# Performance work log

Hardware: AMD Instinct MI355X
Metric: run time of the kernel (lower is better)

Reference implementation:

```python
import jax, jax.numpy as jnp
import numpy as np

N_LAST = 4096  # power of two; K=1 path of get_hadK


def fwht(x):
    """Fast Walsh-Hadamard transform along the last dim, normalized by 1/sqrt(n).
    Matches QuaRot matmul_hadU butterfly recursion (K=1, power-of-two n)."""
    n = x.shape[-1]
    y = x.reshape(-1, n, 1)  # (B, n, 1)
    while y.shape[1] > 1:
        y = y.reshape(y.shape[0], y.shape[1] // 2, 2, y.shape[2])
        a = y[:, :, 0, :]
        b = y[:, :, 1, :]
        # butterfly: interleave (a+b, a-b) back into the trailing dim
        y = jnp.concatenate([a + b, a - b], axis=-1)  # (B, m/2, 2k)
    return y.reshape(x.shape) * np.float32(1.0 / np.sqrt(n))


def setup_inputs() -> dict:
    key = jax.random.key(0)
    x = jax.random.normal(key, (4, 2048, N_LAST), dtype=jnp.float32)
    return {"x": x}


def reference(x) -> jnp.ndarray:
    # HadamardTransform.forward with do_rotate=True
    dtype = x.dtype
    return fwht(x).astype(dtype)
```

## Files before the change

kernel.cpp:

```cpp
#include <hip/hip_runtime.h>


constexpr int N = 4096;
constexpr int LDS_STRIDE = 17;

__device__ __forceinline__ void wht16(float v[16]) {
#pragma unroll
    for (int m = 1; m < 16; m <<= 1) {
#pragma unroll
        for (int g = 0; g < 16; g += 2 * m) {
#pragma unroll
            for (int k = 0; k < m; ++k) {
                float a = v[g + k];
                float b = v[g + k + m];
                v[g + k]     = a + b;
                v[g + k + m] = a - b;
            }
        }
    }
}

__global__ __launch_bounds__(256, 8) void fwht4096_kernel(const float* __restrict__ in,
                                                          float* __restrict__ out) {
    __shared__ float lds[256 * LDS_STRIDE];

    const int t = threadIdx.x;
    const size_t row = blockIdx.x;
    const float* __restrict__ src = in + row * (size_t)N;
    float* __restrict__ dst = out + row * (size_t)N;

    float v[16];

    {
        const float4* s4 = (const float4*)(src + t * 16);
        float4 f0 = s4[0], f1 = s4[1], f2 = s4[2], f3 = s4[3];
        v[0]=f0.x;  v[1]=f0.y;  v[2]=f0.z;  v[3]=f0.w;
        v[4]=f1.x;  v[5]=f1.y;  v[6]=f1.z;  v[7]=f1.w;
        v[8]=f2.x;  v[9]=f2.y;  v[10]=f2.z; v[11]=f2.w;
        v[12]=f3.x; v[13]=f3.y; v[14]=f3.z; v[15]=f3.w;
    }
    wht16(v);

    {
        const int base = (t >> 4) * (16 * LDS_STRIDE) + (t & 15);
#pragma unroll
        for (int j = 0; j < 16; ++j) lds[base + j * LDS_STRIDE] = v[j];
    }
    __syncthreads();
    {
        const int base = t * LDS_STRIDE;
#pragma unroll
        for (int p = 0; p < 16; ++p) v[p] = lds[base + p];
    }
    wht16(v);
    __syncthreads();

    {
        const int base = (t & 15) * LDS_STRIDE + (t >> 4);
#pragma unroll
        for (int j = 0; j < 16; ++j) lds[base + j * (16 * LDS_STRIDE)] = v[j];
    }
    __syncthreads();
    {
        const int base = t * LDS_STRIDE;
#pragma unroll
        for (int p = 0; p < 16; ++p) v[p] = lds[base + p];
    }
    wht16(v);

    const float scale = 0.015625f;
#pragma unroll
    for (int p = 0; p < 16; ++p) dst[p * 256 + t] = v[p] * scale;
}

extern "C" void kernel_launch(void* const* d_in, const int* in_sizes, int n_in,
                              void* d_out, int out_size, void* d_ws, size_t ws_size,
                              hipStream_t stream) {
    const float* x = (const float*)d_in[0];
    float* y = (float*)d_out;
    const int rows = in_sizes[0] / N;
    fwht4096_kernel<<<rows, 256, 0, stream>>>(x, y);
}
```

Baseline: 227.6 us.

## Restructure FWHT as 64x64 factorization with one wave per row

Replaces the three-stage radix-16 decomposition with 256 threads by a two-stage radix-64 decomposition where a single 64-lane wave handles each row with 64 values per thread. This removes one LDS transpose and two barriers, and loads are strided so each lane gathers a column. The cost is much higher register pressure, fewer threads per row, and output stores where each lane writes a contiguous 256-byte chunk, which coalesces less well across the wave.

```diff
diff --git a/kernel.cpp b/kernel.cpp
--- a/kernel.cpp
+++ b/kernel.cpp
@@ -2,13 +2,13 @@
 
 
 constexpr int N = 4096;
-constexpr int LDS_STRIDE = 17;
+constexpr int PAD = 65;
 
-__device__ __forceinline__ void wht16(float v[16]) {
+__device__ __forceinline__ void wht64(float v[64]) {
 #pragma unroll
-    for (int m = 1; m < 16; m <<= 1) {
+    for (int m = 1; m < 64; m <<= 1) {
 #pragma unroll
-        for (int g = 0; g < 16; g += 2 * m) {
+        for (int g = 0; g < 64; g += 2 * m) {
 #pragma unroll
             for (int k = 0; k < m; ++k) {
                 float a = v[g + k];
@@ -20,57 +20,43 @@
     }
 }
 
-__global__ __launch_bounds__(256, 8) void fwht4096_kernel(const float* __restrict__ in,
-                                                          float* __restrict__ out) {
-    __shared__ float lds[256 * LDS_STRIDE];
+__global__ __launch_bounds__(64, 2) void fwht4096_kernel(const float* __restrict__ in,
+                                                         float* __restrict__ out) {
+    __shared__ float lds[64 * PAD];
 
-    const int t = threadIdx.x;
+    const int l = threadIdx.x;
     const size_t row = blockIdx.x;
     const float* __restrict__ src = in + row * (size_t)N;
     float* __restrict__ dst = out + row * (size_t)N;
 
-    float v[16];
+    float v[64];
+
+#pragma unroll
+    for (int j = 0; j < 64; ++j) v[j] = src[j * 64 + l];
+
+    wht64(v);
 
     {
-        const float4* s4 = (const float4*)(src + t * 16);
-        float4 f0 = s4[0], f1 = s4[1], f2 = s4[2], f3 = s4[3];
-        v[0]=f0.x;  v[1]=f0.y;  v[2]=f0.z;  v[3]=f0.w;
-        v[4]=f1.x;  v[5]=f1.y;  v[6]=f1.z;  v[7]=f1.w;
-        v[8]=f2.x;  v[9]=f2.y;  v[10]=f2.z; v[11]=f2.w;
-        v[12]=f3.x; v[13]=f3.y; v[14]=f3.z; v[15]=f3.w;
-    }
-    wht16(v);
-
-    {
-        const int base = (t >> 4) * (16 * LDS_STRIDE) + (t & 15);
+        const int wbase = l;
 #pragma unroll
-        for (int j = 0; j < 16; ++j) lds[base + j * LDS_STRIDE] = v[j];
+        for (int j = 0; j < 64; ++j) lds[wbase + j * PAD] = v[j];
     }
     __syncthreads();
     {
-        const int base = t * LDS_STRIDE;
+        const int rbase = l * PAD;
 #pragma unroll
-        for (int p = 0; p < 16; ++p) v[p] = lds[base + p];
+        for (int k = 0; k < 64; ++k) v[k] = lds[rbase + k];
     }
-    wht16(v);
-    __syncthreads();
 
-    {
-        const int base = (t & 15) * LDS_STRIDE + (t >> 4);
-#pragma unroll
-        for (int j = 0; j < 16; ++j) lds[base + j * (16 * LDS_STRIDE)] = v[j];
-    }
-    __syncthreads();
-    {
-        const int base = t * LDS_STRIDE;
-#pragma unroll
-        for (int p = 0; p < 16; ++p) v[p] = lds[base + p];
-    }
-    wht16(v);
+    wht64(v);
 
     const float scale = 0.015625f;
+    float4* __restrict__ d4 = (float4*)(dst + l * 64);
 #pragma unroll
-    for (int p = 0; p < 16; ++p) dst[p * 256 + t] = v[p] * scale;
+    for (int r = 0; r < 16; ++r) {
+        d4[r] = make_float4(v[4 * r + 0] * scale, v[4 * r + 1] * scale,
+                            v[4 * r + 2] * scale, v[4 * r + 3] * scale);
+    }
 }
 
 extern "C" void kernel_launch(void* const* d_in, const int* in_sizes, int n_in,
@@ -79,5 +65,5 @@
     const float* x = (const float*)d_in[0];
     float* y = (float*)d_out;
     const int rows = in_sizes[0] / N;
-    fwht4096_kernel<<<rows, 256, 0, stream>>>(x, y);
+    fwht4096_kernel<<<rows, 64, 0, stream>>>(x, y);
 }
```

Result: slower. 250.6 us (+10.1%).

## Persistent blocks with double-buffered async global-to-LDS row prefetch

Applied to the files above, without the earlier changes.

Replaces the one-block-per-row launch with a fixed grid of persistent blocks that loop over rows. The next row is prefetched into a second LDS buffer with global_load_lds while the current row is transformed, so load latency overlaps compute. The butterfly passes are reordered so the final output is written as contiguous float4 stores. This raises LDS usage per block and lowers occupancy (launch bounds 3), and it relies on hand-placed waitcnt and barrier instructions for correctness.

```diff
diff --git a/kernel.cpp b/kernel.cpp
--- a/kernel.cpp
+++ b/kernel.cpp
@@ -2,7 +2,8 @@
 
 
 constexpr int N = 4096;
-constexpr int LDS_STRIDE = 17;
+constexpr int SCR_STRIDE = 17;
+constexpr int GRID = 768;
 
 __device__ __forceinline__ void wht16(float v[16]) {
 #pragma unroll
@@ -20,57 +21,94 @@
     }
 }
 
-__global__ __launch_bounds__(256, 8) void fwht4096_kernel(const float* __restrict__ in,
-                                                          float* __restrict__ out) {
-    __shared__ float lds[256 * LDS_STRIDE];
+__device__ __forceinline__ void stage_row(const float* __restrict__ src,
+                                          float* lbuf, int t) {
+    const int w = t >> 6;
+    const int l = t & 63;
+    const float* gp = src + w * 1024 + l * 4;
+    float* lp = lbuf + w * 1024;
+#pragma unroll
+    for (int k = 0; k < 4; ++k) {
+        __builtin_amdgcn_global_load_lds(
+            (const __attribute__((address_space(1))) unsigned int*)(gp + k * 256),
+            (__attribute__((address_space(3))) unsigned int*)(lp + k * 256),
+            16, 0, 0);
+    }
+}
+
+__global__ __launch_bounds__(256, 3) void fwht4096_kernel(const float* __restrict__ in,
+                                                          float* __restrict__ out,
+                                                          int rows) {
+    __shared__ float buf[2][4096];
+    __shared__ float scr[256 * SCR_STRIDE];
 
     const int t = threadIdx.x;
-    const size_t row = blockIdx.x;
-    const float* __restrict__ src = in + row * (size_t)N;
-    float* __restrict__ dst = out + row * (size_t)N;
+    int r = blockIdx.x;
+    if (r >= rows) return;
+    int cur = 0;
 
-    float v[16];
+    stage_row(in + (size_t)r * N, buf[0], t);
+    asm volatile("s_waitcnt vmcnt(0)" ::: "memory");
+    __builtin_amdgcn_s_barrier();
 
-    {
-        const float4* s4 = (const float4*)(src + t * 16);
-        float4 f0 = s4[0], f1 = s4[1], f2 = s4[2], f3 = s4[3];
-        v[0]=f0.x;  v[1]=f0.y;  v[2]=f0.z;  v[3]=f0.w;
-        v[4]=f1.x;  v[5]=f1.y;  v[6]=f1.z;  v[7]=f1.w;
-        v[8]=f2.x;  v[9]=f2.y;  v[10]=f2.z; v[11]=f2.w;
-        v[12]=f3.x; v[13]=f3.y; v[14]=f3.z; v[15]=f3.w;
+    while (r < rows) {
+        const int nxt = r + GRID;
+        if (nxt < rows) stage_row(in + (size_t)nxt * N, buf[cur ^ 1], t);
+        asm volatile("" ::: "memory");
+
+        float v[16];
+        const float* bc = buf[cur];
+
+#pragma unroll
+        for (int j = 0; j < 16; ++j) v[j] = bc[j * 256 + t];
+        wht16(v);
+
+        {
+            const int base = (t & 15) * SCR_STRIDE + (t >> 4);
+#pragma unroll
+            for (int j = 0; j < 16; ++j) scr[base + j * 16 * SCR_STRIDE] = v[j];
+        }
+        asm volatile("s_waitcnt lgkmcnt(0)" ::: "memory");
+        __builtin_amdgcn_s_barrier();
+        {
+            const int base = t * SCR_STRIDE;
+#pragma unroll
+            for (int p = 0; p < 16; ++p) v[p] = scr[base + p];
+        }
+        wht16(v);
+        asm volatile("s_waitcnt lgkmcnt(0)" ::: "memory");
+        __builtin_amdgcn_s_barrier();
+
+        {
+            const int base = (t >> 4) * 16 * SCR_STRIDE + (t & 15);
+#pragma unroll
+            for (int p = 0; p < 16; ++p) scr[base + p * SCR_STRIDE] = v[p];
+        }
+        asm volatile("s_waitcnt lgkmcnt(0)" ::: "memory");
+        __builtin_amdgcn_s_barrier();
+        {
+            const int base = t * SCR_STRIDE;
+#pragma unroll
+            for (int p = 0; p < 16; ++p) v[p] = scr[base + p];
+        }
+        wht16(v);
+
+        {
+            const float scale = 0.015625f;
+            float4* d4 = (float4*)(out + (size_t)r * N + t * 16);
+#pragma unroll
+            for (int q = 0; q < 4; ++q)
+                d4[q] = make_float4(v[4 * q + 0] * scale, v[4 * q + 1] * scale,
+                                    v[4 * q + 2] * scale, v[4 * q + 3] * scale);
+        }
+
+        r = nxt;
+        cur ^= 1;
+        if (r < rows) {
+            asm volatile("s_waitcnt vmcnt(4) lgkmcnt(0)" ::: "memory");
+            __builtin_amdgcn_s_barrier();
+        }
     }
-    wht16(v);
-
-    {
-        const int base = (t >> 4) * (16 * LDS_STRIDE) + (t & 15);
-#pragma unroll
-        for (int j = 0; j < 16; ++j) lds[base + j * LDS_STRIDE] = v[j];
-    }
-    __syncthreads();
-    {
-        const int base = t * LDS_STRIDE;
-#pragma unroll
-        for (int p = 0; p < 16; ++p) v[p] = lds[base + p];
-    }
-    wht16(v);
-    __syncthreads();
-
-    {
-        const int base = (t & 15) * LDS_STRIDE + (t >> 4);
-#pragma unroll
-        for (int j = 0; j < 16; ++j) lds[base + j * (16 * LDS_STRIDE)] = v[j];
-    }
-    __syncthreads();
-    {
-        const int base = t * LDS_STRIDE;
-#pragma unroll
-        for (int p = 0; p < 16; ++p) v[p] = lds[base + p];
-    }
-    wht16(v);
-
-    const float scale = 0.015625f;
-#pragma unroll
-    for (int p = 0; p < 16; ++p) dst[p * 256 + t] = v[p] * scale;
 }
 
 extern "C" void kernel_launch(void* const* d_in, const int* in_sizes, int n_in,
@@ -79,5 +117,5 @@
     const float* x = (const float*)d_in[0];
     float* y = (float*)d_out;
     const int rows = in_sizes[0] / N;
-    fwht4096_kernel<<<rows, 256, 0, stream>>>(x, y);
+    fwht4096_kernel<<<GRID, 256, 0, stream>>>(x, y, rows);
 }
```

Measured after the change: 232.8 us. 2.3% more time.
